# Performance work log

Measured on AMD Instinct MI355X. Metric: run time of the kernel, lower is better.

## Reference

```python
import jax, jax.numpy as jnp
import numpy as np

N_HEAD = 16
N_KV_HEAD = 4
N_EMBD = 2048
HEAD_DIM = N_EMBD // N_HEAD  # 128
RMS_EPS = float(np.finfo(np.float32).eps)  # torch F.rms_norm default eps


def _apply_rotary(x, cos, sin):
    # x: [B,T,H,D]; cos/sin: [1,T,1,D/2]
    d = x.shape[-1] // 2
    x1, x2 = x[..., :d], x[..., d:]
    y1 = x1 * cos + x2 * sin
    y2 = -x1 * sin + x2 * cos
    return jnp.concatenate([y1, y2], axis=-1)


def _rms_norm(x):
    var = jnp.mean(jnp.square(x), axis=-1, keepdims=True)
    return x * jax.lax.rsqrt(var + RMS_EPS)


def setup_inputs() -> dict:
    key = jax.random.key(0)
    ks = jax.random.split(key, 7)
    B, T = 2, 2048
    x = jax.random.normal(ks[0], (B, T, N_EMBD), dtype=jnp.float32)
    cos = jax.random.normal(ks[1], (1, T, 1, HEAD_DIM // 2), dtype=jnp.float32)
    sin = jax.random.normal(ks[2], (1, T, 1, HEAD_DIM // 2), dtype=jnp.float32)
    s = 1.0 / np.sqrt(N_EMBD)
    Wq = jax.random.normal(ks[3], (N_HEAD * HEAD_DIM, N_EMBD), dtype=jnp.float32) * s
    Wk = jax.random.normal(ks[4], (N_KV_HEAD * HEAD_DIM, N_EMBD), dtype=jnp.float32) * s
    Wv = jax.random.normal(ks[5], (N_KV_HEAD * HEAD_DIM, N_EMBD), dtype=jnp.float32) * s
    Wo = jax.random.normal(ks[6], (N_EMBD, N_EMBD), dtype=jnp.float32) * s
    return {"x": x, "cos": cos, "sin": sin, "Wq": Wq, "Wk": Wk, "Wv": Wv, "Wo": Wo}


def reference(x, cos, sin, Wq, Wk, Wv, Wo):
    B, T, C = x.shape
    q = (x @ Wq.T).reshape(B, T, N_HEAD, HEAD_DIM)
    k = (x @ Wk.T).reshape(B, T, N_KV_HEAD, HEAD_DIM)
    v = (x @ Wv.T).reshape(B, T, N_KV_HEAD, HEAD_DIM)
    q = _rms_norm(_apply_rotary(q, cos, sin))
    k = _rms_norm(_apply_rotary(k, cos, sin))
    # to [B,H,T,D]; expand kv heads for GQA
    q = q.transpose(0, 2, 1, 3)
    k = k.transpose(0, 2, 1, 3)
    v = v.transpose(0, 2, 1, 3)
    g = N_HEAD // N_KV_HEAD
    k = jnp.repeat(k, g, axis=1)
    v = jnp.repeat(v, g, axis=1)
    scale = 1.0 / np.sqrt(HEAD_DIM)
    scores = jnp.einsum("bhtd,bhsd->bhts", q, k) * scale
    causal = jnp.tril(jnp.ones((T, T), dtype=bool))
    scores = jnp.where(causal, scores, -jnp.inf)
    attn = jax.nn.softmax(scores, axis=-1)
    y = jnp.einsum("bhts,bhsd->bhtd", attn, v)
    y = y.transpose(0, 2, 1, 3).reshape(B, T, C)
    return y @ Wo.T
```

## Files before the change

### kernel.cpp

```cpp
#include <hip/hip_runtime.h>
#include <hip/hip_bf16.h>
#include <stdint.h>

#define B_   2
#define T_   2048
#define CEMB 2048
#define H_   16
#define HKV_ 4
#define D_   128

typedef __attribute__((ext_vector_type(8))) short bf16x8;
typedef __attribute__((ext_vector_type(4))) float f32x4;
typedef __attribute__((ext_vector_type(16))) float f32x16;

#if __has_builtin(__builtin_amdgcn_exp2f)
#define EXP2(x) __builtin_amdgcn_exp2f(x)
#else
#define EXP2(x) exp2f(x)
#endif

__device__ __forceinline__ unsigned short f2b(float f) {
  union { float f; unsigned u; } v; v.f = f;
  unsigned r = v.u + 0x7FFFu + ((v.u >> 16) & 1u);
  return (unsigned short)(r >> 16);
}
__device__ __forceinline__ float b2f(unsigned short u) {
  union { unsigned u; float f; } v; v.u = ((unsigned)u) << 16; return v.f;
}
__device__ __forceinline__ unsigned cvtpk(float lo, float hi) {
  unsigned r;
  asm("v_cvt_pk_bf16_f32 %0, %1, %2" : "=v"(r) : "v"(lo), "v"(hi));
  return r;
}

#if __has_builtin(__builtin_amdgcn_permlane32_swap)
__device__ __forceinline__ void pl32(unsigned& a, unsigned& b) {
  auto r = __builtin_amdgcn_permlane32_swap(a, b, false, false);
  a = r[0]; b = r[1];
}
#else
__device__ __forceinline__ void pl32(unsigned& a, unsigned& b) {
  const bool hih = (threadIdx.x & 32) != 0;
  unsigned sa = __shfl_xor(a, 32), sb = __shfl_xor(b, 32);
  unsigned na = hih ? sb : a;
  unsigned nb = hih ? b : sa;
  a = na; b = nb;
}
#endif

__device__ __forceinline__ void gl16(const void* g, void* l) {
  __builtin_amdgcn_global_load_lds(
      (const __attribute__((address_space(1))) unsigned int*)g,
      (__attribute__((address_space(3))) unsigned int*)l, 16, 0, 0);
}

#define FENCE() asm volatile("" ::: "memory")

__global__ void cvt_kernel(const float* __restrict__ src,
                           unsigned short* __restrict__ dst, int n4) {
  int i = blockIdx.x * blockDim.x + threadIdx.x;
  const int stride = gridDim.x * blockDim.x;
  for (; i < n4; i += stride) {
    float4 v = ((const float4*)src)[i];
    ushort4 o;
    o.x = f2b(v.x); o.y = f2b(v.y); o.z = f2b(v.z); o.w = f2b(v.w);
    ((ushort4*)dst)[i] = o;
  }
}

__global__ __launch_bounds__(512, 2)
void gemm256(const unsigned short* __restrict__ A,
             const unsigned short* __restrict__ W,
             void* __restrict__ Cmat, int M, int N, int K, int obf16) {
  __shared__ alignas(16) unsigned short As[2][2][128][64];
  __shared__ alignas(16) unsigned short Bs[2][2][128][64];

  const int tid  = threadIdx.x;
  const int lane = tid & 63;
  const int w    = tid >> 6;
  const int wr   = w >> 2;
  const int wc   = w & 3;
  const int l16  = lane & 15, g4 = lane >> 4;
  const int srow = lane >> 3;
  const int schk = lane & 7;

  const int gx  = gridDim.x;
  const int nwg = gx * gridDim.y;
  const int lin = blockIdx.y * gx + blockIdx.x;
  const int cpx = nwg >> 3;
  const int swz = (lin & 7) * cpx + (lin >> 3);
  const int m0 = (swz / gx) * 256;
  const int n0 = (swz % gx) * 256;

  const unsigned short* Ap = A + (size_t)m0 * K;
  const unsigned short* Wp = W + (size_t)n0 * K;
  const int nk = K >> 6;

  f32x4 acc[8][4] = {};

  auto stA = [&](int ts, int h) {
    const unsigned short* g = Ap + (size_t)(h * 128 + w * 8 + srow) * K
                                 + ts * 64 + ((schk ^ srow) << 3);
    unsigned short* l = &As[ts & 1][h][w * 8][0];
    gl16(g, l);
    gl16(g + (size_t)64 * K, l + 64 * 64);
  };
  auto stB = [&](int ts, int h) {
    const unsigned short* g = Wp + (size_t)(h * 128 + w * 8 + srow) * K
                                 + ts * 64 + ((schk ^ srow) << 3);
    unsigned short* l = &Bs[ts & 1][h][w * 8][0];
    gl16(g, l);
    gl16(g + (size_t)64 * K, l + 64 * 64);
  };

  stA(0, 0); stB(0, 0); stA(0, 1); stB(0, 1);
  stA(1, 0); stB(1, 0);
  asm volatile("s_waitcnt vmcnt(4)" ::: "memory");
  __builtin_amdgcn_s_barrier();
  FENCE();

  for (int tau = 0; tau < nk; ++tau) {
    const int buf = tau & 1;
    bf16x8 af[4][2], bf0[2][2], bf1[2][2];
    #pragma unroll
    for (int mi = 0; mi < 4; ++mi) {
      const int har = (mi * 2 + wr) * 16 + l16;
      #pragma unroll
      for (int ks = 0; ks < 2; ++ks)
        af[mi][ks] = *(const bf16x8*)&As[buf][0][har][((ks * 4 + g4) ^ (l16 & 7)) << 3];
    }
    #pragma unroll
    for (int ni = 0; ni < 2; ++ni) {
      const int hbr = (ni * 4 + wc) * 16 + l16;
      #pragma unroll
      for (int ks = 0; ks < 2; ++ks)
        bf0[ni][ks] = *(const bf16x8*)&Bs[buf][0][hbr][((ks * 4 + g4) ^ (l16 & 7)) << 3];
    }
    if (tau + 1 < nk) stA(tau + 1, 1);
    __builtin_amdgcn_s_setprio(1);
    #pragma unroll
    for (int mi = 0; mi < 4; ++mi) {
      #pragma unroll
      for (int ni = 0; ni < 2; ++ni) {
        f32x4 t = acc[mi][ni];
        t = __builtin_amdgcn_mfma_f32_16x16x32_bf16(af[mi][0], bf0[ni][0], t, 0, 0, 0);
        t = __builtin_amdgcn_mfma_f32_16x16x32_bf16(af[mi][1], bf0[ni][1], t, 0, 0, 0);
        acc[mi][ni] = t;
      }
    }
    __builtin_amdgcn_s_setprio(0);
    __builtin_amdgcn_s_barrier();
    FENCE();
    #pragma unroll
    for (int ni = 0; ni < 2; ++ni) {
      const int hbr = (ni * 4 + wc) * 16 + l16;
      #pragma unroll
      for (int ks = 0; ks < 2; ++ks)
        bf1[ni][ks] = *(const bf16x8*)&Bs[buf][1][hbr][((ks * 4 + g4) ^ (l16 & 7)) << 3];
    }
    if (tau + 1 < nk) stB(tau + 1, 1);
    __builtin_amdgcn_s_setprio(1);
    #pragma unroll
    for (int mi = 0; mi < 4; ++mi) {
      #pragma unroll
      for (int ni = 0; ni < 2; ++ni) {
        f32x4 t = acc[mi][2 + ni];
        t = __builtin_amdgcn_mfma_f32_16x16x32_bf16(af[mi][0], bf1[ni][0], t, 0, 0, 0);
        t = __builtin_amdgcn_mfma_f32_16x16x32_bf16(af[mi][1], bf1[ni][1], t, 0, 0, 0);
        acc[mi][2 + ni] = t;
      }
    }
    __builtin_amdgcn_s_setprio(0);
    __builtin_amdgcn_s_barrier();
    FENCE();
    #pragma unroll
    for (int mi = 0; mi < 4; ++mi) {
      const int har = (mi * 2 + wr) * 16 + l16;
      #pragma unroll
      for (int ks = 0; ks < 2; ++ks)
        af[mi][ks] = *(const bf16x8*)&As[buf][1][har][((ks * 4 + g4) ^ (l16 & 7)) << 3];
    }
    if (tau + 2 < nk) stA(tau + 2, 0);
    __builtin_amdgcn_s_setprio(1);
    #pragma unroll
    for (int mi = 0; mi < 4; ++mi) {
      #pragma unroll
      for (int ni = 0; ni < 2; ++ni) {
        f32x4 t = acc[4 + mi][2 + ni];
        t = __builtin_amdgcn_mfma_f32_16x16x32_bf16(af[mi][0], bf1[ni][0], t, 0, 0, 0);
        t = __builtin_amdgcn_mfma_f32_16x16x32_bf16(af[mi][1], bf1[ni][1], t, 0, 0, 0);
        acc[4 + mi][2 + ni] = t;
      }
    }
    __builtin_amdgcn_s_setprio(0);
    __builtin_amdgcn_s_barrier();
    FENCE();
    if (tau + 2 < nk) stB(tau + 2, 0);
    __builtin_amdgcn_s_setprio(1);
    #pragma unroll
    for (int mi = 0; mi < 4; ++mi) {
      #pragma unroll
      for (int ni = 0; ni < 2; ++ni) {
        f32x4 t = acc[4 + mi][ni];
        t = __builtin_amdgcn_mfma_f32_16x16x32_bf16(af[mi][0], bf0[ni][0], t, 0, 0, 0);
        t = __builtin_amdgcn_mfma_f32_16x16x32_bf16(af[mi][1], bf0[ni][1], t, 0, 0, 0);
        acc[4 + mi][ni] = t;
      }
    }
    __builtin_amdgcn_s_setprio(0);
    if (tau + 2 < nk) asm volatile("s_waitcnt vmcnt(4)" ::: "memory");
    else              asm volatile("s_waitcnt vmcnt(0)" ::: "memory");
    __builtin_amdgcn_s_barrier();
    FENCE();
  }

  #pragma unroll
  for (int fr = 0; fr < 8; ++fr) {
    #pragma unroll
    for (int fc = 0; fc < 4; ++fc) {
      const int row = m0 + (fr * 2 + wr) * 16 + g4 * 4;
      const int col = n0 + (fc * 4 + wc) * 16 + l16;
      if (obf16) {
        unsigned short* Cb = (unsigned short*)Cmat;
        #pragma unroll
        for (int r = 0; r < 4; ++r)
          Cb[(size_t)(row + r) * N + col] = f2b(acc[fr][fc][r]);
      } else {
        float* Cf = (float*)Cmat;
        #pragma unroll
        for (int r = 0; r < 4; ++r)
          Cf[(size_t)(row + r) * N + col] = acc[fr][fc][r];
      }
    }
  }
}

__global__ __launch_bounds__(128)
void rope_norm(const unsigned short* __restrict__ X, int rstride,
               const float* __restrict__ Cos, const float* __restrict__ Sin,
               unsigned short* __restrict__ Out, int Hn, float out_scale) {
  const int idx = blockIdx.x;
  const int h  = idx % Hn;
  const int bt = idx / Hn;
  const int t  = bt & (T_ - 1);
  const int b  = bt >> 11;
  const int d  = threadIdx.x;
  const unsigned short* src = X + (size_t)bt * rstride + h * D_;
  float y;
  if (d < 64) {
    float x1 = b2f(src[d]), x2 = b2f(src[d + 64]);
    float c = Cos[t * 64 + d], s = Sin[t * 64 + d];
    y = x1 * c + x2 * s;
  } else {
    int dd = d - 64;
    float x1 = b2f(src[dd]), x2 = b2f(src[d]);
    float c = Cos[t * 64 + dd], s = Sin[t * 64 + dd];
    y = -x1 * s + x2 * c;
  }
  float ss = y * y;
  #pragma unroll
  for (int m = 32; m; m >>= 1) ss += __shfl_xor(ss, m);
  __shared__ float red[2];
  if ((d & 63) == 0) red[d >> 6] = ss;
  __syncthreads();
  const float tot  = red[0] + red[1];
  const float rinv = rsqrtf(tot * (1.0f / 128.0f) + 1.1920929e-7f) * out_scale;
  Out[(((size_t)b * Hn + h) * T_ + t) * D_ + d] = f2b(y * rinv);
}

__global__ __launch_bounds__(256)
void vtrans(const unsigned short* __restrict__ Vf, int rstride,
            unsigned short* __restrict__ Vt) {
  __shared__ float tile[32][65];
  const int t0 = blockIdx.x * 64;
  const int d0 = blockIdx.y * 32;
  const int bh = blockIdx.z;
  const int b = bh >> 2, hk = bh & 3;
  const int tid = threadIdx.x;
  {
    const int di = tid & 31, ts = tid >> 5;
    #pragma unroll
    for (int i = 0; i < 8; ++i) {
      int tt = ts + i * 8;
      tile[di][tt] = b2f(Vf[(size_t)(b * T_ + t0 + tt) * rstride + hk * D_ + d0 + di]);
    }
  }
  __syncthreads();
  {
    const int ti = tid & 63, ds = tid >> 6;
    #pragma unroll
    for (int i = 0; i < 8; ++i) {
      int dd = ds * 8 + i;
      Vt[((size_t)bh * D_ + d0 + dd) * T_ + t0 + ti] = f2b(tile[dd][ti]);
    }
  }
}

#define KVB 128

__global__ __launch_bounds__(512)
void attn_kernel(const unsigned short* __restrict__ Qn,
                 const unsigned short* __restrict__ Kn,
                 const unsigned short* __restrict__ Vt,
                 unsigned short* __restrict__ Yb) {
  __shared__ alignas(16) unsigned short Ks[2][KVB][D_];
  __shared__ alignas(16) unsigned short Vs[2][D_][KVB];

  const int tid = threadIdx.x;
  const int lane = tid & 63;
  const int w = tid >> 6;
  const int wq  = w & 3;
  const int kvg = w >> 2;
  const int l31 = lane & 31;
  const int hi  = lane >> 5;
  const int bh = blockIdx.x;
  const int by = blockIdx.y;
  const int qt = (by < 8) ? by : 23 - by;
  const int b = bh >> 4, h = bh & 15;
  const int hk = h >> 2;

  const unsigned short* kp = Kn + ((size_t)(b * HKV_ + hk) * T_) * D_;
  const unsigned short* vp = Vt + ((size_t)(b * HKV_ + hk) * D_) * T_;

  const int r4 = lane >> 4, c16 = lane & 15;

  const int t0 = qt * 128;
  const int qrow0 = t0 + wq * 32;
  const int qmax = qrow0 + 31;
  const int nt = qt + 1;
  const int qglob = qrow0 + l31;

  const unsigned short* qp = Qn + ((size_t)bh * T_ + qrow0) * D_;
  bf16x8 qf[8];
  #pragma unroll
  for (int ds = 0; ds < 8; ++ds)
    qf[ds] = *(const bf16x8*)(qp + (size_t)l31 * D_ + ds * 16 + hi * 8);

  f32x16 o[4] = {};
  float l_lane = 0.f;

  auto stage = [&](int tt) {
    const int buf = tt & 1;
    const int kv = tt * KVB;
    #pragma unroll
    for (int j = 0; j < 4; ++j) {
      const int row = w * 16 + j * 4 + r4;
      const int cg = c16 ^ (row & 7);
      gl16(kp + (size_t)(kv + row) * D_ + cg * 8, &Ks[buf][w * 16 + j * 4][0]);
    }
    #pragma unroll
    for (int j = 0; j < 4; ++j) {
      const int row = w * 16 + j * 4 + r4;
      const int cg = c16 ^ (row & 7);
      gl16(vp + (size_t)row * T_ + kv + cg * 8, &Vs[buf][w * 16 + j * 4][0]);
    }
  };

  stage(0);

  union PAu { unsigned u[4]; bf16x8 v; };

  for (int t = 0; t < nt; ++t) {
    __syncthreads();
    if (t + 1 < nt) stage(t + 1);
    const int kbase = t * KVB + kvg * 64;
    if (kbase <= qmax) {
      const unsigned short (*kb)[D_]  = Ks[t & 1];
      const unsigned short (*vbp)[KVB] = Vs[t & 1];
      f32x16 s0 = {}, s1 = {};
      #pragma unroll
      for (int ds = 0; ds < 8; ++ds) {
        const int key0 = kvg * 64 + l31;
        const int key1 = kvg * 64 + 32 + l31;
        bf16x8 k0 = *(const bf16x8*)&kb[key0][(((ds * 2 + hi) ^ (key0 & 7)) << 3)];
        bf16x8 k1 = *(const bf16x8*)&kb[key1][(((ds * 2 + hi) ^ (key1 & 7)) << 3)];
        s0 = __builtin_amdgcn_mfma_f32_32x32x16_bf16(k0, qf[ds], s0, 0, 0, 0);
        s1 = __builtin_amdgcn_mfma_f32_32x32x16_bf16(k1, qf[ds], s1, 0, 0, 0);
      }
      const bool need_mask = (kbase + 63 > qrow0);
      float e0[16], e1[16];
      float ls = 0.f;
      #pragma unroll
      for (int r = 0; r < 16; ++r) {
        const int crow = (r & 3) + 8 * (r >> 2) + 4 * hi;
        float v0 = EXP2(s0[r]);
        float v1 = EXP2(s1[r]);
        if (need_mask) {
          v0 = (kbase + crow      <= qglob) ? v0 : 0.f;
          v1 = (kbase + 32 + crow <= qglob) ? v1 : 0.f;
        }
        e0[r] = v0; e1[r] = v1;
        ls += v0 + v1;
      }
      l_lane += ls;
      PAu pa[4];
      {
        unsigned a0 = cvtpk(e0[0],  e0[1]),  a1 = cvtpk(e0[2],  e0[3]);
        unsigned b0 = cvtpk(e0[4],  e0[5]),  b1 = cvtpk(e0[6],  e0[7]);
        unsigned c0 = cvtpk(e0[8],  e0[9]),  c1 = cvtpk(e0[10], e0[11]);
        unsigned d0 = cvtpk(e0[12], e0[13]), d1 = cvtpk(e0[14], e0[15]);
        pl32(a0, b0); pl32(a1, b1); pl32(c0, d0); pl32(c1, d1);
        pa[0].u[0] = a0; pa[0].u[1] = a1; pa[0].u[2] = b0; pa[0].u[3] = b1;
        pa[1].u[0] = c0; pa[1].u[1] = c1; pa[1].u[2] = d0; pa[1].u[3] = d1;
      }
      {
        unsigned a0 = cvtpk(e1[0],  e1[1]),  a1 = cvtpk(e1[2],  e1[3]);
        unsigned b0 = cvtpk(e1[4],  e1[5]),  b1 = cvtpk(e1[6],  e1[7]);
        unsigned c0 = cvtpk(e1[8],  e1[9]),  c1 = cvtpk(e1[10], e1[11]);
        unsigned d0 = cvtpk(e1[12], e1[13]), d1 = cvtpk(e1[14], e1[15]);
        pl32(a0, b0); pl32(a1, b1); pl32(c0, d0); pl32(c1, d1);
        pa[2].u[0] = a0; pa[2].u[1] = a1; pa[2].u[2] = b0; pa[2].u[3] = b1;
        pa[3].u[0] = c0; pa[3].u[1] = c1; pa[3].u[2] = d0; pa[3].u[3] = d1;
      }
      #pragma unroll
      for (int ks = 0; ks < 4; ++ks) {
        #pragma unroll
        for (int db = 0; db < 4; ++db) {
          const int d = db * 32 + l31;
          const int c = (kvg * 8 + ks * 2 + hi) ^ (d & 7);
          bf16x8 vf = *(const bf16x8*)&vbp[d][c << 3];
          o[db] = __builtin_amdgcn_mfma_f32_32x32x16_bf16(pa[ks].v, vf, o[db], 0, 0, 0);
        }
      }
    }
  }

  const float lfull = l_lane + __shfl_xor(l_lane, 32);
  __syncthreads();
  float* obuf = (float*)&Ks[0][0][0];
  float* lbuf = (float*)&Vs[0][0][0];
  if (w >= 4) {
    const int base = (w - 4) * 4096;
    #pragma unroll
    for (int r = 0; r < 16; ++r)
      #pragma unroll
      for (int db = 0; db < 4; ++db)
        obuf[base + (r * 4 + db) * 64 + lane] = o[db][r];
    if (hi == 0) lbuf[(w - 4) * 32 + l31] = lfull;
  }
  __syncthreads();
  if (w < 4) {
    const int base = w * 4096;
    const float ltot = lfull + lbuf[w * 32 + l31];
    const float invq = 1.0f / ltot;
    #pragma unroll
    for (int r = 0; r < 16; ++r) {
      const int crow = (r & 3) + 8 * (r >> 2) + 4 * hi;
      const float inv = __shfl(invq, crow);
      unsigned short* yrow = Yb + ((size_t)(b * T_ + qrow0 + crow) * CEMB) + h * D_;
      #pragma unroll
      for (int db = 0; db < 4; ++db)
        yrow[db * 32 + l31] = f2b((o[db][r] + obuf[base + (r * 4 + db) * 64 + lane]) * inv);
    }
  }
}

extern "C" void kernel_launch(void* const* d_in, const int* in_sizes, int n_in,
                              void* d_out, int out_size, void* d_ws, size_t ws_size,
                              hipStream_t stream) {
  const float* x    = (const float*)d_in[0];
  const float* cosp = (const float*)d_in[1];
  const float* sinp = (const float*)d_in[2];
  const float* Wq   = (const float*)d_in[3];
  const float* Wk   = (const float*)d_in[4];
  const float* Wv   = (const float*)d_in[5];
  const float* Wo   = (const float*)d_in[6];
  float* out = (float*)d_out;

  char* ws = (char*)d_ws;
  size_t off = 0;
  auto alloc = [&](size_t bytes) {
    void* p = ws + off;
    off += (bytes + 255) & ~(size_t)255;
    return p;
  };
  const size_t MT = (size_t)B_ * T_;
  const int NQKV = 3072;
  unsigned short* xb    = (unsigned short*)alloc(MT * CEMB * 2);
  unsigned short* wqkvb = (unsigned short*)alloc((size_t)NQKV * 2048 * 2);
  unsigned short* wob   = (unsigned short*)alloc((size_t)2048 * 2048 * 2);
  unsigned short* qkvb  = (unsigned short*)alloc(MT * NQKV * 2);
  unsigned short* qn    = (unsigned short*)alloc((size_t)B_ * H_ * T_ * D_ * 2);
  unsigned short* kn    = (unsigned short*)alloc((size_t)B_ * HKV_ * T_ * D_ * 2);
  unsigned short* vt    = (unsigned short*)alloc((size_t)B_ * HKV_ * D_ * T_ * 2);
  unsigned short* yb    = (unsigned short*)alloc(MT * CEMB * 2);

  cvt_kernel<<<2048, 256, 0, stream>>>(x,  xb, (int)(MT * CEMB / 4));
  cvt_kernel<<<1024, 256, 0, stream>>>(Wq, wqkvb,                2048 * 2048 / 4);
  cvt_kernel<<<256,  256, 0, stream>>>(Wk, wqkvb + 2048 * 2048,  512 * 2048 / 4);
  cvt_kernel<<<256,  256, 0, stream>>>(Wv, wqkvb + 2560 * 2048,  512 * 2048 / 4);
  cvt_kernel<<<1024, 256, 0, stream>>>(Wo, wob,                  2048 * 2048 / 4);

  gemm256<<<dim3(NQKV / 256, 4096 / 256), 512, 0, stream>>>(xb, wqkvb, qkvb, 4096, NQKV, 2048, 1);

  rope_norm<<<4096 * H_,   128, 0, stream>>>(qkvb,        NQKV, cosp, sinp, qn, H_,   0.1275174324f);
  rope_norm<<<4096 * HKV_, 128, 0, stream>>>(qkvb + 2048, NQKV, cosp, sinp, kn, HKV_, 1.0f);
  vtrans<<<dim3(T_ / 64, D_ / 32, B_ * HKV_), 256, 0, stream>>>(qkvb + 2560, NQKV, vt);

  attn_kernel<<<dim3(B_ * H_, 16), 512, 0, stream>>>(qn, kn, vt, yb);

  gemm256<<<dim3(2048 / 256, 4096 / 256), 512, 0, stream>>>(yb, wob, out, 4096, 2048, 2048, 0);
}
```

Measured before the change: 220.1 us.

## Use 256x128-tile GEMM kernel for output projection to double workgroup count

Adds a specialized GEMM kernel with 256x128 output tiles, split-half A staging, a pipelined LDS double buffer and XCD-aware block swizzling, and uses it for the Wo projection. The previous 256x256 tiling launched only 128 workgroups on a GPU with 256 CUs. The new one launches 256 and allows two blocks per CU via launch bounds. The trade-off is less reuse of A per tile and more global traffic for A.

```diff
diff --git a/kernel.cpp b/kernel.cpp
--- a/kernel.cpp
+++ b/kernel.cpp
@@ -231,6 +231,132 @@
         for (int r = 0; r < 4; ++r)
           Cf[(size_t)(row + r) * N + col] = acc[fr][fc][r];
       }
+    }
+  }
+}
+
+__global__ __launch_bounds__(512, 2)
+void gemm_n128(const unsigned short* __restrict__ A,
+               const unsigned short* __restrict__ W,
+               float* __restrict__ Cmat, int M, int N, int K) {
+  __shared__ alignas(16) unsigned short As[2][2][128][64];
+  __shared__ alignas(16) unsigned short Bs[2][2][64][64];
+
+  const int tid  = threadIdx.x;
+  const int lane = tid & 63;
+  const int w    = tid >> 6;
+  const int wr   = w >> 2;
+  const int wc   = w & 3;
+  const int l16  = lane & 15, g4 = lane >> 4;
+  const int srow = lane >> 3;
+  const int schk = lane & 7;
+
+  const int gx  = gridDim.x;
+  const int nwg = gx * gridDim.y;
+  const int lin = blockIdx.y * gx + blockIdx.x;
+  const int cpx = nwg >> 3;
+  const int swz = (lin & 7) * cpx + (lin >> 3);
+  const int m0 = (swz / gx) * 256;
+  const int n0 = (swz % gx) * 128;
+
+  const unsigned short* Ap = A + (size_t)m0 * K;
+  const unsigned short* Wp = W + (size_t)n0 * K;
+  const int nk = K >> 6;
+
+  const int bh_ = wc >> 1;
+  const int br0 = (wc & 1) * 32;
+
+  f32x4 acc[8][2] = {};
+
+  auto stA = [&](int ts, int h) {
+    const unsigned short* g = Ap + (size_t)(h * 128 + w * 8 + srow) * K
+                                 + ts * 64 + ((schk ^ srow) << 3);
+    unsigned short* l = &As[ts & 1][h][w * 8][0];
+    gl16(g, l);
+    gl16(g + (size_t)64 * K, l + 64 * 64);
+  };
+  auto stB = [&](int ts, int h) {
+    const unsigned short* g = Wp + (size_t)(h * 64 + w * 8 + srow) * K
+                                 + ts * 64 + ((schk ^ srow) << 3);
+    gl16(g, &Bs[ts & 1][h][w * 8][0]);
+  };
+
+  stA(0, 0); stA(0, 1); stB(0, 0); stB(0, 1);
+  stA(1, 0); stB(1, 0); stB(1, 1);
+  asm volatile("s_waitcnt vmcnt(4)" ::: "memory");
+  __builtin_amdgcn_s_barrier();
+  FENCE();
+
+  for (int t = 0; t < nk; ++t) {
+    const int buf = t & 1;
+    bf16x8 af[4][2], bfr[2][2];
+    #pragma unroll
+    for (int mi = 0; mi < 4; ++mi) {
+      const int har = (mi * 2 + wr) * 16 + l16;
+      #pragma unroll
+      for (int ks = 0; ks < 2; ++ks)
+        af[mi][ks] = *(const bf16x8*)&As[buf][0][har][((ks * 4 + g4) ^ (l16 & 7)) << 3];
+    }
+    #pragma unroll
+    for (int fc = 0; fc < 2; ++fc) {
+      const int br = br0 + fc * 16 + l16;
+      #pragma unroll
+      for (int ks = 0; ks < 2; ++ks)
+        bfr[fc][ks] = *(const bf16x8*)&Bs[buf][bh_][br][((ks * 4 + g4) ^ (l16 & 7)) << 3];
+    }
+    if (t + 1 < nk) stA(t + 1, 1);
+    __builtin_amdgcn_s_setprio(1);
+    #pragma unroll
+    for (int mi = 0; mi < 4; ++mi) {
+      #pragma unroll
+      for (int fc = 0; fc < 2; ++fc) {
+        f32x4 a = acc[mi][fc];
+        a = __builtin_amdgcn_mfma_f32_16x16x32_bf16(af[mi][0], bfr[fc][0], a, 0, 0, 0);
+        a = __builtin_amdgcn_mfma_f32_16x16x32_bf16(af[mi][1], bfr[fc][1], a, 0, 0, 0);
+        acc[mi][fc] = a;
+      }
+    }
+    __builtin_amdgcn_s_setprio(0);
+    if (t + 2 < nk) asm volatile("s_waitcnt vmcnt(6)" ::: "memory");
+    else            asm volatile("s_waitcnt vmcnt(0)" ::: "memory");
+    __builtin_amdgcn_s_barrier();
+    FENCE();
+    #pragma unroll
+    for (int mi = 0; mi < 4; ++mi) {
+      const int har = (mi * 2 + wr) * 16 + l16;
+      #pragma unroll
+      for (int ks = 0; ks < 2; ++ks)
+        af[mi][ks] = *(const bf16x8*)&As[buf][1][har][((ks * 4 + g4) ^ (l16 & 7)) << 3];
+    }
+    if (t + 2 < nk) { stA(t + 2, 0); stB(t + 2, 0); stB(t + 2, 1); }
+    __builtin_amdgcn_s_setprio(1);
+    #pragma unroll
+    for (int mi = 0; mi < 4; ++mi) {
+      #pragma unroll
+      for (int fc = 0; fc < 2; ++fc) {
+        f32x4 a = acc[4 + mi][fc];
+        a = __builtin_amdgcn_mfma_f32_16x16x32_bf16(af[mi][0], bfr[fc][0], a, 0, 0, 0);
+        a = __builtin_amdgcn_mfma_f32_16x16x32_bf16(af[mi][1], bfr[fc][1], a, 0, 0, 0);
+        acc[4 + mi][fc] = a;
+      }
+    }
+    __builtin_amdgcn_s_setprio(0);
+    if (t + 2 < nk) asm volatile("s_waitcnt vmcnt(6)" ::: "memory");
+    else            asm volatile("s_waitcnt vmcnt(0)" ::: "memory");
+    __builtin_amdgcn_s_barrier();
+    FENCE();
+  }
+
+  #pragma unroll
+  for (int fr = 0; fr < 8; ++fr) {
+    const int hh = fr >> 2, mi = fr & 3;
+    #pragma unroll
+    for (int fc = 0; fc < 2; ++fc) {
+      const int row = m0 + hh * 128 + (mi * 2 + wr) * 16 + g4 * 4;
+      const int col = n0 + wc * 32 + fc * 16 + l16;
+      #pragma unroll
+      for (int r = 0; r < 4; ++r)
+        Cmat[(size_t)(row + r) * N + col] = acc[fr][fc][r];
     }
   }
 }
@@ -499,5 +625,5 @@
 
   attn_kernel<<<dim3(B_ * H_, 16), 512, 0, stream>>>(qn, kn, vt, yb);
 
-  gemm256<<<dim3(2048 / 256, 4096 / 256), 512, 0, stream>>>(yb, wob, out, 4096, 2048, 2048, 0);
-}
+  gemm_n128<<<dim3(2048 / 128, 4096 / 256), 512, 0, stream>>>(yb, wob, out, 4096, 2048, 2048);
+}
```

Result: faster. 203.0 us (-7.8%).
